# Optimization experiments

Measured on AMD Instinct MI355X. Metric: run time of the kernel, lower is better.

The kernel has to match this reference:

```python
import jax, jax.numpy as jnp
import numpy as np

SIZE = 512
NUM_NODES = 32
BATCH = 8192
EPS = 1e-5  # torch LayerNorm default eps


def setup_inputs() -> dict:
    key = jax.random.key(0)
    k1, k2 = jax.random.split(key)
    x = jax.random.normal(k1, (BATCH, NUM_NODES), dtype=jnp.float32)
    # xavier_uniform_ for Linear(1, SIZE): bound = sqrt(6/(1+SIZE))
    bound = float(np.sqrt(6.0 / (1 + SIZE)))
    w = jax.random.uniform(k2, (SIZE,), dtype=jnp.float32, minval=-bound, maxval=bound)
    b = jnp.zeros((SIZE,), dtype=jnp.float32)
    gamma = jnp.ones((SIZE,), dtype=jnp.float32)
    beta = jnp.zeros((SIZE,), dtype=jnp.float32)
    return {"x": x, "w": w, "b": b, "gamma": gamma, "beta": beta}


def reference(x, w, b, gamma, beta):
    scale = jnp.sqrt(jnp.asarray(SIZE, dtype=x.dtype))
    # Broadcast scalar->vector projection (collapses the per-node python loop)
    # h: (batch, num_nodes, size)
    h = (x[:, :, None] * w + b) * scale
    # LayerNorm over the last dim (biased variance, like torch.nn.LayerNorm)
    mean = jnp.mean(h, axis=-1, keepdims=True)
    var = jnp.mean(jnp.square(h - mean), axis=-1, keepdims=True)
    out = (h - mean) * jax.lax.rsqrt(var + EPS) * gamma + beta
    # dropout is identity in eval mode
    return out
```

## Files before the change

kernel.cpp:

```cpp
#include <hip/hip_runtime.h>

#define LN_SIZE 512
#define LN_ROWS (8192 * 32)
#define LN_EPS 1e-5f
#define LN_SCALE 22.62741699796952f
#define RPW 32

typedef float f32x4 __attribute__((ext_vector_type(4)));

__global__ __launch_bounds__(256) void ln_fused_kernel(
    const float* __restrict__ x, const float* __restrict__ w,
    const float* __restrict__ b, const float* __restrict__ gamma,
    const float* __restrict__ beta, float* __restrict__ out) {
  const int tid  = (int)threadIdx.x;
  const int lane = tid & 63;
  const int wv   = tid >> 6;

  float sw, sb, sww, swb, sbb;
  {
    const int j0 = tid, j1 = tid + 256;
    const float w0 = w[j0], w1 = w[j1];
    const float p0 = b[j0], p1 = b[j1];
    sw  = w0 + w1;
    sb  = p0 + p1;
    sww = w0 * w0 + w1 * w1;
    swb = w0 * p0 + w1 * p1;
    sbb = p0 * p0 + p1 * p1;
  }
#pragma unroll
  for (int off = 32; off > 0; off >>= 1) {
    sw  += __shfl_xor(sw, off);
    sb  += __shfl_xor(sb, off);
    sww += __shfl_xor(sww, off);
    swb += __shfl_xor(swb, off);
    sbb += __shfl_xor(sbb, off);
  }
  __shared__ float red[4][5];
  if (lane == 0) {
    red[wv][0] = sw; red[wv][1] = sb; red[wv][2] = sww;
    red[wv][3] = swb; red[wv][4] = sbb;
  }
  __syncthreads();
  sw  = red[0][0] + red[1][0] + red[2][0] + red[3][0];
  sb  = red[0][1] + red[1][1] + red[2][1] + red[3][1];
  sww = red[0][2] + red[1][2] + red[2][2] + red[3][2];
  swb = red[0][3] + red[1][3] + red[2][3] + red[3][3];
  sbb = red[0][4] + red[1][4] + red[2][4] + red[3][4];

  const float inv_n = 1.0f / (float)LN_SIZE;
  const float mw  = sw * inv_n;
  const float mb  = sb * inv_n;
  const float Sww = sww * inv_n - mw * mw;
  const float Swb = swb * inv_n - mw * mb;
  const float Sbb = sbb * inv_n - mb * mb;
  const float c2 = (float)LN_SIZE * Sww;
  const float c1 = 2.0f * (float)LN_SIZE * Swb;
  const float c0 = (float)LN_SIZE * Sbb;

  const int j = lane * 8;
  const float4 wv0 = *(const float4*)(w + j);
  const float4 wv1 = *(const float4*)(w + j + 4);
  const float4 bv0 = *(const float4*)(b + j);
  const float4 bv1 = *(const float4*)(b + j + 4);
  const float4 gv0 = *(const float4*)(gamma + j);
  const float4 gv1 = *(const float4*)(gamma + j + 4);
  const float4 g0  = *(const float4*)(beta + j);
  const float4 g1  = *(const float4*)(beta + j + 4);

  float4 a0, a1, B0, B1;
  a0.x = (wv0.x - mw) * gv0.x;  a0.y = (wv0.y - mw) * gv0.y;
  a0.z = (wv0.z - mw) * gv0.z;  a0.w = (wv0.w - mw) * gv0.w;
  a1.x = (wv1.x - mw) * gv1.x;  a1.y = (wv1.y - mw) * gv1.y;
  a1.z = (wv1.z - mw) * gv1.z;  a1.w = (wv1.w - mw) * gv1.w;
  B0.x = (bv0.x - mb) * gv0.x;  B0.y = (bv0.y - mb) * gv0.y;
  B0.z = (bv0.z - mb) * gv0.z;  B0.w = (bv0.w - mb) * gv0.w;
  B1.x = (bv1.x - mb) * gv1.x;  B1.y = (bv1.y - mb) * gv1.y;
  B1.z = (bv1.z - mb) * gv1.z;  B1.w = (bv1.w - mb) * gv1.w;

  const int wid  = (int)((blockIdx.x * blockDim.x + tid) >> 6);
  const int row0 = wid * RPW;
  if (row0 >= LN_ROWS) return;

  const float xv  = x[row0 + (lane & 31)];
  const float var = fmaf(fmaf(c2, xv, c1), xv, c0);
  const float rv  = LN_SCALE * rsqrtf(var + LN_EPS);

  float* dst = out + (size_t)row0 * LN_SIZE + j;
#pragma unroll
  for (int i = 0; i < RPW; ++i) {
    const float xi = __shfl(xv, i);
    const float ri = __shfl(rv, i);

    f32x4 o0, o1;
    o0.x = fmaf(fmaf(xi, a0.x, B0.x), ri, g0.x);
    o0.y = fmaf(fmaf(xi, a0.y, B0.y), ri, g0.y);
    o0.z = fmaf(fmaf(xi, a0.z, B0.z), ri, g0.z);
    o0.w = fmaf(fmaf(xi, a0.w, B0.w), ri, g0.w);
    o1.x = fmaf(fmaf(xi, a1.x, B1.x), ri, g1.x);
    o1.y = fmaf(fmaf(xi, a1.y, B1.y), ri, g1.y);
    o1.z = fmaf(fmaf(xi, a1.z, B1.z), ri, g1.z);
    o1.w = fmaf(fmaf(xi, a1.w, B1.w), ri, g1.w);

    *(f32x4*)(dst)     = o0;
    *(f32x4*)(dst + 4) = o1;
    dst += LN_SIZE;
  }
}

extern "C" void kernel_launch(void* const* d_in, const int* in_sizes, int n_in,
                              void* d_out, int out_size, void* d_ws, size_t ws_size,
                              hipStream_t stream) {
  const float* x     = (const float*)d_in[0];
  const float* w     = (const float*)d_in[1];
  const float* b     = (const float*)d_in[2];
  const float* gamma = (const float*)d_in[3];
  const float* beta  = (const float*)d_in[4];
  float* out = (float*)d_out;
  (void)d_ws; (void)ws_size;

  ln_fused_kernel<<<2048, 256, 0, stream>>>(x, w, b, gamma, beta, out);
}
```

Before: 100.6 us.

## Interleave rows across waves and compute weight stats per wave without LDS sync

Each wave now handles rows g, g+8192, ... instead of 32 contiguous rows, so at any moment all waves write adjacent 2KB rows and the write stream is spread across the output differently. The weight/bias statistics are computed per wave from the already-loaded float4 vectors with a wave shuffle reduction, which removes the shared-memory reduction and __syncthreads. The row-bound check is dropped. The x read becomes strided across lanes (stride 8192 floats), which is uncoalesced but small.

Measured after the change: 112.7 us. 11.9% more time.

```diff
diff --git a/kernel.cpp b/kernel.cpp
--- a/kernel.cpp
+++ b/kernel.cpp
@@ -1,6 +1,7 @@
 #include <hip/hip_runtime.h>
 
 #define LN_SIZE 512
+#define LN_NWAVES 8192
 #define LN_ROWS (8192 * 32)
 #define LN_EPS 1e-5f
 #define LN_SCALE 22.62741699796952f
@@ -14,19 +15,28 @@
     const float* __restrict__ beta, float* __restrict__ out) {
   const int tid  = (int)threadIdx.x;
   const int lane = tid & 63;
-  const int wv   = tid >> 6;
+  const int g    = (int)((blockIdx.x * blockDim.x + tid) >> 6);
+  const int j    = lane * 8;
 
-  float sw, sb, sww, swb, sbb;
-  {
-    const int j0 = tid, j1 = tid + 256;
-    const float w0 = w[j0], w1 = w[j1];
-    const float p0 = b[j0], p1 = b[j1];
-    sw  = w0 + w1;
-    sb  = p0 + p1;
-    sww = w0 * w0 + w1 * w1;
-    swb = w0 * p0 + w1 * p1;
-    sbb = p0 * p0 + p1 * p1;
-  }
+  const float xv = x[g + LN_NWAVES * (lane & 31)];
+
+  const float4 wv0 = *(const float4*)(w + j);
+  const float4 wv1 = *(const float4*)(w + j + 4);
+  const float4 bv0 = *(const float4*)(b + j);
+  const float4 bv1 = *(const float4*)(b + j + 4);
+  const float4 gv0 = *(const float4*)(gamma + j);
+  const float4 gv1 = *(const float4*)(gamma + j + 4);
+  const float4 g0  = *(const float4*)(beta + j);
+  const float4 g1  = *(const float4*)(beta + j + 4);
+
+  float sw  = wv0.x + wv0.y + wv0.z + wv0.w + wv1.x + wv1.y + wv1.z + wv1.w;
+  float sb  = bv0.x + bv0.y + bv0.z + bv0.w + bv1.x + bv1.y + bv1.z + bv1.w;
+  float sww = wv0.x*wv0.x + wv0.y*wv0.y + wv0.z*wv0.z + wv0.w*wv0.w
+            + wv1.x*wv1.x + wv1.y*wv1.y + wv1.z*wv1.z + wv1.w*wv1.w;
+  float swb = wv0.x*bv0.x + wv0.y*bv0.y + wv0.z*bv0.z + wv0.w*bv0.w
+            + wv1.x*bv1.x + wv1.y*bv1.y + wv1.z*bv1.z + wv1.w*bv1.w;
+  float sbb = bv0.x*bv0.x + bv0.y*bv0.y + bv0.z*bv0.z + bv0.w*bv0.w
+            + bv1.x*bv1.x + bv1.y*bv1.y + bv1.z*bv1.z + bv1.w*bv1.w;
 #pragma unroll
   for (int off = 32; off > 0; off >>= 1) {
     sw  += __shfl_xor(sw, off);
@@ -35,17 +45,6 @@
     swb += __shfl_xor(swb, off);
     sbb += __shfl_xor(sbb, off);
   }
-  __shared__ float red[4][5];
-  if (lane == 0) {
-    red[wv][0] = sw; red[wv][1] = sb; red[wv][2] = sww;
-    red[wv][3] = swb; red[wv][4] = sbb;
-  }
-  __syncthreads();
-  sw  = red[0][0] + red[1][0] + red[2][0] + red[3][0];
-  sb  = red[0][1] + red[1][1] + red[2][1] + red[3][1];
-  sww = red[0][2] + red[1][2] + red[2][2] + red[3][2];
-  swb = red[0][3] + red[1][3] + red[2][3] + red[3][3];
-  sbb = red[0][4] + red[1][4] + red[2][4] + red[3][4];
 
   const float inv_n = 1.0f / (float)LN_SIZE;
   const float mw  = sw * inv_n;
@@ -57,16 +56,6 @@
   const float c1 = 2.0f * (float)LN_SIZE * Swb;
   const float c0 = (float)LN_SIZE * Sbb;
 
-  const int j = lane * 8;
-  const float4 wv0 = *(const float4*)(w + j);
-  const float4 wv1 = *(const float4*)(w + j + 4);
-  const float4 bv0 = *(const float4*)(b + j);
-  const float4 bv1 = *(const float4*)(b + j + 4);
-  const float4 gv0 = *(const float4*)(gamma + j);
-  const float4 gv1 = *(const float4*)(gamma + j + 4);
-  const float4 g0  = *(const float4*)(beta + j);
-  const float4 g1  = *(const float4*)(beta + j + 4);
-
   float4 a0, a1, B0, B1;
   a0.x = (wv0.x - mw) * gv0.x;  a0.y = (wv0.y - mw) * gv0.y;
   a0.z = (wv0.z - mw) * gv0.z;  a0.w = (wv0.w - mw) * gv0.w;
@@ -77,15 +66,10 @@
   B1.x = (bv1.x - mb) * gv1.x;  B1.y = (bv1.y - mb) * gv1.y;
   B1.z = (bv1.z - mb) * gv1.z;  B1.w = (bv1.w - mb) * gv1.w;
 
-  const int wid  = (int)((blockIdx.x * blockDim.x + tid) >> 6);
-  const int row0 = wid * RPW;
-  if (row0 >= LN_ROWS) return;
-
-  const float xv  = x[row0 + (lane & 31)];
   const float var = fmaf(fmaf(c2, xv, c1), xv, c0);
   const float rv  = LN_SCALE * rsqrtf(var + LN_EPS);
 
-  float* dst = out + (size_t)row0 * LN_SIZE + j;
+  float* dst = out + (size_t)g * LN_SIZE + j;
 #pragma unroll
   for (int i = 0; i < RPW; ++i) {
     const float xi = __shfl(xv, i);
@@ -103,7 +87,7 @@
 
     *(f32x4*)(dst)     = o0;
     *(f32x4*)(dst + 4) = o1;
-    dst += LN_SIZE;
+    dst += (size_t)LN_NWAVES * LN_SIZE;
   }
 }
 
```
